# Kernel optimization log

Measured on AMD Instinct MI355X. Metric: run time of the kernel, lower is better.

The kernel has to match this reference:

```python
import jax, jax.numpy as jnp
import numpy as np
from jax import lax

HEADS = 4
DIM = 64
GATE_HID = 16


def setup_inputs() -> dict:
    key = jax.random.key(0)
    ks = jax.random.split(key, 12)
    b, c, h, w = 2, DIM, 48, 48
    s = 0.05
    x = jax.random.normal(ks[0], (b, c, h, w), jnp.float32)
    Wqkv = jax.random.normal(ks[1], (3 * c, c), jnp.float32) * s
    bqkv = jax.random.normal(ks[2], (3 * c,), jnp.float32) * s
    Wpos = jax.random.normal(ks[3], (3 * c, 1, 3, 3), jnp.float32) * s
    bpos = jax.random.normal(ks[4], (3 * c,), jnp.float32) * s
    Wg1 = jax.random.normal(ks[5], (GATE_HID, 1), jnp.float32) * 0.5
    bg1 = jax.random.normal(ks[6], (GATE_HID,), jnp.float32) * 0.1
    Wg2 = jax.random.normal(ks[7], (1, GATE_HID), jnp.float32) * 0.5
    bg2 = jax.random.normal(ks[8], (1,), jnp.float32) * 0.1
    Wproj = jax.random.normal(ks[9], (c, c), jnp.float32) * s
    bproj = jax.random.normal(ks[10], (c,), jnp.float32) * s
    return {"x": x, "Wqkv": Wqkv, "bqkv": bqkv, "Wpos": Wpos, "bpos": bpos,
            "Wg1": Wg1, "bg1": bg1, "Wg2": Wg2, "bg2": bg2,
            "Wproj": Wproj, "bproj": bproj}


def _forward(x, Wqkv, bqkv, Wpos, bpos, Wg1, bg1, Wg2, bg2, Wproj, bproj):
    b, c, h, w = x.shape
    n = h * w
    heads = HEADS
    hd = c // heads
    scale = hd ** -0.5
    # qkv 1x1 conv then 3x3 depthwise positional conv
    qkv = jnp.einsum('bchw,oc->bohw', x, Wqkv) + bqkv[None, :, None, None]
    qkv = lax.conv_general_dilated(
        qkv, Wpos, window_strides=(1, 1), padding='SAME',
        feature_group_count=3 * c,
        dimension_numbers=('NCHW', 'OIHW', 'NCHW')) + bpos[None, :, None, None]
    q, k, v = jnp.split(qkv, 3, axis=1)

    def to_heads(t):
        # [b,c,h,w] -> [b,heads,n,hd]
        return t.reshape(b, c, n).transpose(0, 2, 1).reshape(b, n, heads, hd).transpose(0, 2, 1, 3)

    q, k, v = to_heads(q), to_heads(k), to_heads(v)
    attn = jnp.einsum('bhid,bhjd->bhij', q, k) * scale  # [b,heads,n,n]
    prob = jax.nn.softmax(attn, axis=-1)
    entropy = -(prob * jnp.log(jnp.clip(prob, 1e-12))).sum(-1).mean(-1)  # [b,heads]
    # entropy gate: sigmoid(fc2(relu(fc1(e)))) * 0.9 + 0.1
    hgate = jax.nn.relu(entropy[..., None] @ Wg1.T + bg1)  # [b,heads,16]
    ratio = jax.nn.sigmoid(hgate @ Wg2.T + bg2)[..., 0] * 0.9 + 0.1  # [b,heads]
    # dynamic per-(batch,head) top-k along rows via rank threshold
    keep = jnp.clip(jnp.ceil(ratio * n).astype(jnp.int32), 1, n)  # [b,heads]
    sorted_desc = -jnp.sort(-attn, axis=-1)  # [b,heads,n,n]
    idx = jnp.broadcast_to((keep - 1)[:, :, None, None], (b, heads, n, 1))
    thresh = jnp.take_along_axis(sorted_desc, idx, axis=-1)  # [b,heads,n,1]
    sparse = jnp.where(attn >= thresh, attn, -jnp.inf)
    p = jax.nn.softmax(sparse, axis=-1)
    out = jnp.einsum('bhij,bhjd->bhid', p, v)  # [b,heads,n,hd]
    out = out.transpose(0, 2, 1, 3).reshape(b, n, c)
    out = out @ Wproj.T + bproj
    return out.transpose(0, 2, 1).reshape(b, c, h, w)


def reference(x, Wqkv, bqkv, Wpos, bpos, Wg1, bg1, Wg2, bg2, Wproj, bproj):
    return _forward(x, Wqkv, bqkv, Wpos, bpos, Wg1, bg1, Wg2, bg2, Wproj, bproj)
```

## Files before the change

kernel.cpp:

```cpp
#include <hip/hip_runtime.h>
#include <hip/hip_fp16.h>


#define NEG_INF (-__builtin_huge_valf())

typedef _Float16 half8_t __attribute__((ext_vector_type(8)));
typedef float floatx4 __attribute__((ext_vector_type(4)));

__device__ __forceinline__ unsigned h2key(unsigned short u) {
  return (u & 0x8000u) ? (unsigned)((~u) & 0xFFFFu) : (unsigned)(u | 0x8000u);
}
__device__ __forceinline__ float key16_to_float(unsigned k) {
  unsigned short u = (k & 0x8000u) ? (unsigned short)(k & 0x7FFFu)
                                   : (unsigned short)((~k) & 0xFFFFu);
  return __half2float(__ushort_as_half(u));
}

__device__ __forceinline__ float max8(uint4 v, float mx) {
  float2 f0 = __half22float2(*(__half2*)&v.x);
  float2 f1 = __half22float2(*(__half2*)&v.y);
  float2 f2 = __half22float2(*(__half2*)&v.z);
  float2 f3 = __half22float2(*(__half2*)&v.w);
  mx = fmaxf(mx, fmaxf(fmaxf(f0.x, f0.y), fmaxf(f1.x, f1.y)));
  mx = fmaxf(mx, fmaxf(fmaxf(f2.x, f2.y), fmaxf(f3.x, f3.y)));
  return mx;
}

__device__ __forceinline__ uint4 maskExp8(uint4 v, float th, float m,
                                          float& sp) {
  float2 f0 = __half22float2(*(__half2*)&v.x);
  float2 f1 = __half22float2(*(__half2*)&v.y);
  float2 f2 = __half22float2(*(__half2*)&v.z);
  float2 f3 = __half22float2(*(__half2*)&v.w);
  float p0 = (f0.x >= th) ? __expf(f0.x - m) : 0.f;
  float p1 = (f0.y >= th) ? __expf(f0.y - m) : 0.f;
  float p2 = (f1.x >= th) ? __expf(f1.x - m) : 0.f;
  float p3 = (f1.y >= th) ? __expf(f1.y - m) : 0.f;
  float p4 = (f2.x >= th) ? __expf(f2.x - m) : 0.f;
  float p5 = (f2.y >= th) ? __expf(f2.y - m) : 0.f;
  float p6 = (f3.x >= th) ? __expf(f3.x - m) : 0.f;
  float p7 = (f3.y >= th) ? __expf(f3.y - m) : 0.f;
  sp += ((p0 + p1) + (p2 + p3)) + ((p4 + p5) + (p6 + p7));
  uint4 o;
  __half2 h0 = __floats2half2_rn(p0, p1); o.x = *(unsigned*)&h0;
  __half2 h1 = __floats2half2_rn(p2, p3); o.y = *(unsigned*)&h1;
  __half2 h2 = __floats2half2_rn(p4, p5); o.z = *(unsigned*)&h2;
  __half2 h3 = __floats2half2_rn(p6, p7); o.w = *(unsigned*)&h3;
  return o;
}

__global__ __launch_bounds__(256) void k_qkv(const float* __restrict__ x,
                                             const float* __restrict__ W,
                                             const float* __restrict__ bias,
                                             float* __restrict__ out) {
  int blk = blockIdx.x;
  int chunk = blk % 9;
  int o = (blk / 9) % 192;
  int b = blk / (9 * 192);
  int pos = chunk * 256 + threadIdx.x;
  const float* xb = x + b * 64 * 2304 + pos;
  const float* wr = W + o * 64;
  float acc = bias[o];
#pragma unroll
  for (int c = 0; c < 64; c++) acc = fmaf(wr[c], xb[c * 2304], acc);
  out[(b * 192 + o) * 2304 + pos] = acc;
}

__global__ __launch_bounds__(256) void k_dw(const float* __restrict__ qkv,
                                            const float* __restrict__ Wpos,
                                            const float* __restrict__ bpos,
                                            _Float16* __restrict__ q2,
                                            _Float16* __restrict__ k2,
                                            _Float16* __restrict__ vt) {
  int blk = blockIdx.x;
  int chunk = blk % 9;
  int ch = (blk / 9) % 192;
  int b = blk / (9 * 192);
  int pos = chunk * 256 + threadIdx.x;
  int yy = pos / 48, xx = pos % 48;
  const float* in = qkv + (b * 192 + ch) * 2304;
  const float* w = Wpos + ch * 9;
  float acc = bpos[ch];
#pragma unroll
  for (int dy = -1; dy <= 1; dy++) {
    int y2 = yy + dy;
    if ((unsigned)y2 < 48u) {
#pragma unroll
      for (int dx = -1; dx <= 1; dx++) {
        int x2 = xx + dx;
        if ((unsigned)x2 < 48u)
          acc = fmaf(w[(dy + 1) * 3 + (dx + 1)], in[y2 * 48 + x2], acc);
      }
    }
  }
  int sel = ch >> 6;
  int c = ch & 63;
  int head = c >> 4, d = c & 15;
  int bh = b * 4 + head;
  if (sel == 2) {
    vt[((size_t)bh * 16 + d) * 2304 + pos] = (_Float16)acc;
  } else {
    if (sel == 0) acc *= 0.25f;
    size_t idx = (size_t)bh * 2304 + pos;
    _Float16 h1 = (_Float16)acc;
    float r = acc - (float)h1;
    _Float16 h2 = (_Float16)r;
    _Float16* dst = (sel == 0) ? q2 : k2;
    dst[idx * 32 + d] = h1;
    dst[idx * 32 + 16 + d] = h2;
  }
}

template <bool STORE>
__global__ __launch_bounds__(256) void k_ent_t(const _Float16* __restrict__ q2,
                                               const _Float16* __restrict__ k2,
                                               float* __restrict__ ent,
                                               _Float16* __restrict__ lgH) {
  __shared__ __align__(16) _Float16 tBuf[4][16][72];
  __shared__ float mWv[4][16], sWv[4][16], uWv[4][16];

  int blk = blockIdx.x;
  int rowtile = blk % 144;
  int bh = blk / 144;
  int row0 = rowtile * 16;
  int tid = threadIdx.x, lane = tid & 63, wave = tid >> 6;
  int m16 = lane & 15, quad = lane >> 4;

  const half8_t* q2v =
      (const half8_t*)(q2 + ((size_t)bh * 2304 + row0 + m16) * 32);
  half8_t A1 = q2v[quad];
  half8_t zh = {};
  half8_t A2 = (lane < 32) ? A1 : zh;
  const half8_t* kbase = (const half8_t*)(k2 + (size_t)bh * 2304 * 32);

  float mreg[4] = {NEG_INF, NEG_INF, NEG_INF, NEG_INF};
  for (int g = 0; g < 9; g++) {
#pragma unroll
    for (int tt = 0; tt < 4; tt++) {
      int t = g * 4 + tt;
      int col = wave * 576 + t * 16 + m16;
      const half8_t* kk = kbase + (size_t)col * 4;
      half8_t b1 = kk[quad & 1];
      half8_t b2 = kk[2 + (quad & 1)];
      floatx4 acc = {};
      acc = __builtin_amdgcn_mfma_f32_16x16x32_f16(A2, b2, acc, 0, 0, 0);
      acc = __builtin_amdgcn_mfma_f32_16x16x32_f16(A1, b1, acc, 0, 0, 0);
#pragma unroll
      for (int i = 0; i < 4; i++) {
        mreg[i] = fmaxf(mreg[i], acc[i]);
        if (STORE) tBuf[wave][quad * 4 + i][tt * 16 + m16] = (_Float16)acc[i];
      }
    }
    if (STORE) {
      __syncthreads();
      int rb = lane >> 3, seg = lane & 7;
#pragma unroll
      for (int it = 0; it < 2; it++) {
        int rr = it * 8 + rb;
        uint4 vv = *(const uint4*)&tBuf[wave][rr][seg * 8];
        *(uint4*)(lgH + ((size_t)bh * 2304 + row0 + rr) * 2304 + wave * 576 +
                  g * 64 + seg * 8) = vv;
      }
      __syncthreads();
    }
  }
#pragma unroll
  for (int off = 1; off < 16; off <<= 1)
#pragma unroll
    for (int i = 0; i < 4; i++)
      mreg[i] = fmaxf(mreg[i], __shfl_xor(mreg[i], off));
  if (m16 == 0) {
#pragma unroll
    for (int i = 0; i < 4; i++) mWv[wave][quad * 4 + i] = mreg[i];
  }
  __syncthreads();
  float mrow[4];
#pragma unroll
  for (int i = 0; i < 4; i++) {
    int r = quad * 4 + i;
    mrow[i] = fmaxf(fmaxf(mWv[0][r], mWv[1][r]), fmaxf(mWv[2][r], mWv[3][r]));
  }

  float s[4] = {0.f, 0.f, 0.f, 0.f}, u[4] = {0.f, 0.f, 0.f, 0.f};
#pragma unroll 4
  for (int t = 0; t < 36; t++) {
    int col = wave * 576 + t * 16 + m16;
    const half8_t* kk = kbase + (size_t)col * 4;
    half8_t b1 = kk[quad & 1];
    half8_t b2 = kk[2 + (quad & 1)];
    floatx4 acc = {};
    acc = __builtin_amdgcn_mfma_f32_16x16x32_f16(A2, b2, acc, 0, 0, 0);
    acc = __builtin_amdgcn_mfma_f32_16x16x32_f16(A1, b1, acc, 0, 0, 0);
#pragma unroll
    for (int i = 0; i < 4; i++) {
      float z = acc[i] - mrow[i];
      float e = __expf(z);
      s[i] += e;
      u[i] = fmaf(z, e, u[i]);
    }
  }
#pragma unroll
  for (int off = 1; off < 16; off <<= 1) {
#pragma unroll
    for (int i = 0; i < 4; i++) {
      s[i] += __shfl_xor(s[i], off);
      u[i] += __shfl_xor(u[i], off);
    }
  }
  if (m16 == 0) {
#pragma unroll
    for (int i = 0; i < 4; i++) {
      sWv[wave][quad * 4 + i] = s[i];
      uWv[wave][quad * 4 + i] = u[i];
    }
  }
  __syncthreads();
  if (tid < 16) {
    float S = sWv[0][tid] + sWv[1][tid] + sWv[2][tid] + sWv[3][tid];
    float U = uWv[0][tid] + uWv[1][tid] + uWv[2][tid] + uWv[3][tid];
    float er = __logf(S) - U / S;
    er += __shfl_xor(er, 1);
    er += __shfl_xor(er, 2);
    er += __shfl_xor(er, 4);
    er += __shfl_xor(er, 8);
    if (tid == 0) atomicAdd(&ent[bh], er);
  }
}

template <bool CACHED>
__global__ __launch_bounds__(256, 7) void k_attn_t(
    const _Float16* __restrict__ q2, const _Float16* __restrict__ k2,
    const _Float16* __restrict__ vt, const _Float16* __restrict__ lgH,
    const float* __restrict__ ent, const float* __restrict__ Wg1,
    const float* __restrict__ bg1, const float* __restrict__ Wg2,
    const float* __restrict__ bg2, float* __restrict__ oh) {
  __shared__ __align__(16) _Float16 pbuf[4][2320];
  __shared__ float sS[4];
  __shared__ float mShF[4][4];
  __shared__ __align__(16) float redSh[4][64];

  int blk = blockIdx.x;
  int rowblk = blk % 576;
  int bh = blk / 576;
  int row0 = rowblk * 4;
  int tid = threadIdx.x, lane = tid & 63, wave = tid >> 6;

  float eAvg = ent[bh] * (1.f / 2304.f);
  float gacc = bg2[0];
#pragma unroll
  for (int i = 0; i < 16; i++) {
    float h = fmaxf(fmaf(eAvg, Wg1[i], bg1[i]), 0.f);
    gacc = fmaf(h, Wg2[i], gacc);
  }
  float ratio = 0.9f / (1.f + __expf(-gacc)) + 0.1f;
  int kp = (int)ceilf(ratio * 2304.f);
  unsigned keep = (unsigned)min(max(kp, 1), 2304);

  float m;
  uint4* dst4 = (uint4*)pbuf[wave];
  if (CACHED) {
    const uint4* src =
        (const uint4*)(lgH + ((size_t)bh * 2304 + row0 + wave) * 2304);
    float mx = NEG_INF;
#pragma unroll
    for (int it = 0; it < 4; it++) {
      int idx = lane + it * 64;
      uint4 v = src[idx];
      dst4[idx] = v;
      mx = max8(v, mx);
    }
    if (lane < 32) {
      uint4 v = src[256 + lane];
      dst4[256 + lane] = v;
      mx = max8(v, mx);
    }
#pragma unroll
    for (int off = 1; off < 64; off <<= 1) mx = fmaxf(mx, __shfl_xor(mx, off));
    m = mx;
  } else {
    int m16 = lane & 15, quad = lane >> 4;
    const half8_t* q2v =
        (const half8_t*)(q2 + ((size_t)bh * 2304 + row0 + (m16 & 3)) * 32);
    half8_t A1 = q2v[quad];
    half8_t zh = {};
    half8_t A2 = (lane < 32) ? A1 : zh;
    const half8_t* kbase = (const half8_t*)(k2 + (size_t)bh * 2304 * 32);
    float ml[4] = {NEG_INF, NEG_INF, NEG_INF, NEG_INF};
#pragma unroll 4
    for (int t = 0; t < 36; t++) {
      int ct = wave * 36 + t;
      int col = ct * 16 + m16;
      const half8_t* kk = kbase + (size_t)col * 4;
      half8_t b1 = kk[quad & 1];
      half8_t b2 = kk[2 + (quad & 1)];
      floatx4 acc = {};
      acc = __builtin_amdgcn_mfma_f32_16x16x32_f16(A2, b2, acc, 0, 0, 0);
      acc = __builtin_amdgcn_mfma_f32_16x16x32_f16(A1, b1, acc, 0, 0, 0);
      if (lane < 16) {
#pragma unroll
        for (int i = 0; i < 4; i++) {
          pbuf[i][ct * 16 + lane] = (_Float16)acc[i];
          ml[i] = fmaxf(ml[i], acc[i]);
        }
      }
    }
#pragma unroll
    for (int off = 1; off < 16; off <<= 1)
#pragma unroll
      for (int i = 0; i < 4; i++) ml[i] = fmaxf(ml[i], __shfl_xor(ml[i], off));
    if (lane == 0) {
#pragma unroll
      for (int i = 0; i < 4; i++) mShF[wave][i] = ml[i];
    }
    __syncthreads();
    m = fmaxf(fmaxf(mShF[0][wave], mShF[1][wave]),
              fmaxf(mShF[2][wave], mShF[3][wave]));
  }

  float th;
  {
    const unsigned short* prow = (const unsigned short*)pbuf[wave];
    unsigned keys[36];
#pragma unroll
    for (int i = 0; i < 36; i++) keys[i] = h2key(prow[lane + i * 64]);
    unsigned T = 0u;
    for (int bit = 15; bit >= 0; --bit) {
      unsigned cand = T | (1u << bit);
      unsigned cnt = 0u;
#pragma unroll
      for (int i = 0; i < 36; i++)
        cnt += (unsigned)__popcll(__ballot(keys[i] >= cand));
      if (cnt >= keep) {
        T = cand;
        if (cnt == keep) break;
      }
    }
    th = key16_to_float(T);
  }

  {
    float sp = 0.f;
#pragma unroll
    for (int it = 0; it < 4; it++) {
      int idx = lane + it * 64;
      dst4[idx] = maskExp8(dst4[idx], th, m, sp);
    }
    if (lane < 32) {
      int idx = 256 + lane;
      dst4[idx] = maskExp8(dst4[idx], th, m, sp);
    }
#pragma unroll
    for (int off = 1; off < 64; off <<= 1) sp += __shfl_xor(sp, off);
    if (lane == 0) sS[wave] = sp;
  }
  __syncthreads();

  {
    int m16 = lane & 15, quad = lane >> 4;
    const _Float16* vrow = vt + ((size_t)bh * 16 + m16) * 2304;
    const _Float16* prow = pbuf[m16 & 3];
    int jb0 = wave * 576 + quad * 8;
    floatx4 acc = {};
#pragma unroll 6
    for (int t = 0; t < 18; t++) {
      int jb = jb0 + t * 32;
      half8_t a = *(const half8_t*)&prow[jb];
      half8_t b = *(const half8_t*)&vrow[jb];
      acc = __builtin_amdgcn_mfma_f32_16x16x32_f16(a, b, acc, 0, 0, 0);
    }
    if (lane < 16) {
      *(floatx4*)&redSh[wave][m16 * 4] = acc;
    }
  }
  __syncthreads();
  if (tid < 64) {
    int r = tid & 3, d = tid >> 2;
    float s2 = redSh[0][d * 4 + r] + redSh[1][d * 4 + r] +
               redSh[2][d * 4 + r] + redSh[3][d * 4 + r];
    oh[((size_t)(bh * 2304 + row0 + r)) * 16 + d] = s2 / sS[r];
  }
}

__global__ __launch_bounds__(256) void k_proj(const float* __restrict__ oh,
                                              const float* __restrict__ Wp,
                                              const float* __restrict__ bp,
                                              float* __restrict__ out) {
  int blk = blockIdx.x;
  int chunk = blk % 9;
  int co = (blk / 9) % 64;
  int b = blk / (9 * 64);
  int pos = chunk * 256 + threadIdx.x;
  const float* wr = Wp + co * 64;
  float acc = bp[co];
#pragma unroll
  for (int head = 0; head < 4; head++) {
    const float4* op =
        (const float4*)(oh + ((size_t)((b * 4 + head) * 2304 + pos)) * 16);
#pragma unroll
    for (int p = 0; p < 4; p++) {
      float4 o4 = op[p];
      acc = fmaf(wr[head * 16 + p * 4 + 0], o4.x, acc);
      acc = fmaf(wr[head * 16 + p * 4 + 1], o4.y, acc);
      acc = fmaf(wr[head * 16 + p * 4 + 2], o4.z, acc);
      acc = fmaf(wr[head * 16 + p * 4 + 3], o4.w, acc);
    }
  }
  out[(b * 64 + co) * 2304 + pos] = acc;
}

extern "C" void kernel_launch(void* const* d_in, const int* in_sizes, int n_in,
                              void* d_out, int out_size, void* d_ws,
                              size_t ws_size, hipStream_t stream) {
  const float* x    = (const float*)d_in[0];
  const float* Wqkv = (const float*)d_in[1];
  const float* bqkv = (const float*)d_in[2];
  const float* Wpos = (const float*)d_in[3];
  const float* bpos = (const float*)d_in[4];
  const float* Wg1  = (const float*)d_in[5];
  const float* bg1  = (const float*)d_in[6];
  const float* Wg2  = (const float*)d_in[7];
  const float* bg2  = (const float*)d_in[8];
  const float* Wpr  = (const float*)d_in[9];
  const float* bpr  = (const float*)d_in[10];
  float* out = (float*)d_out;

  const size_t lgBytes = (size_t)8 * 2304 * 2304 * 2;
  const size_t baseBytes = (size_t)(884736 + 294912 + 8) * 4 +
                           (size_t)(2 * 589824 + 294912) * 2;
  bool cached = ws_size >= lgBytes + baseBytes;

  char* base = (char*)d_ws;
  _Float16* lgH = nullptr;
  if (cached) {
    lgH = (_Float16*)base;
    base += lgBytes;
  }
  float* qkv_raw = (float*)base;
  float* oh = qkv_raw + 884736;
  float* ent = oh + 294912;
  _Float16* q2 = (_Float16*)(ent + 8);
  _Float16* k2 = q2 + 589824;
  _Float16* vt = k2 + 589824;

  (void)hipMemsetAsync(ent, 0, 8 * sizeof(float), stream);
  hipLaunchKernelGGL(k_qkv, dim3(2 * 192 * 9), dim3(256), 0, stream,
                     x, Wqkv, bqkv, qkv_raw);
  hipLaunchKernelGGL(k_dw, dim3(2 * 192 * 9), dim3(256), 0, stream,
                     qkv_raw, Wpos, bpos, q2, k2, vt);
  if (cached) {
    hipLaunchKernelGGL((k_ent_t<true>), dim3(8 * 144), dim3(256), 0, stream,
                       q2, k2, ent, lgH);
    hipLaunchKernelGGL((k_attn_t<true>), dim3(8 * 576), dim3(256), 0, stream,
                       q2, k2, vt, lgH, ent, Wg1, bg1, Wg2, bg2, oh);
  } else {
    hipLaunchKernelGGL((k_ent_t<false>), dim3(8 * 144), dim3(256), 0, stream,
                       q2, k2, ent, lgH);
    hipLaunchKernelGGL((k_attn_t<false>), dim3(8 * 576), dim3(256), 0, stream,
                       q2, k2, vt, lgH, ent, Wg1, bg1, Wg2, bg2, oh);
  }
  hipLaunchKernelGGL(k_proj, dim3(2 * 64 * 9), dim3(256), 0, stream,
                     oh, Wpr, bpr, out);
}
```

Before: 229.2 us.

## Register-block qkv/proj, tile depthwise conv in LDS, re-read cached logits for entropy

The qkv and projection kernels now compute four output channels per thread, so each loaded input value is reused four times and the grids shrink. The depthwise conv stages a 16-channel row tile in shared memory and writes each q/k position as vectorised 16-byte stores. The entropy memset is folded into the qkv kernel. In the cached path, the entropy pass now re-reads the just-written fp16 logits instead of recomputing them with a second MFMA sweep. The fp16 re-read slightly changes entropy precision, and the smaller grids may leave the GPU underfilled.

New measurement: 245.8 us. 1.07x slower.

```diff
diff --git a/kernel.cpp b/kernel.cpp
--- a/kernel.cpp
+++ b/kernel.cpp
@@ -52,18 +52,34 @@
 __global__ __launch_bounds__(256) void k_qkv(const float* __restrict__ x,
                                              const float* __restrict__ W,
                                              const float* __restrict__ bias,
-                                             float* __restrict__ out) {
+                                             float* __restrict__ out,
+                                             float* __restrict__ ent) {
+  if (blockIdx.x == 0 && threadIdx.x < 8) ent[threadIdx.x] = 0.f;
   int blk = blockIdx.x;
   int chunk = blk % 9;
-  int o = (blk / 9) % 192;
-  int b = blk / (9 * 192);
+  int og = (blk / 9) % 48;
+  int b = blk / (9 * 48);
+  int o0 = og * 4;
   int pos = chunk * 256 + threadIdx.x;
   const float* xb = x + b * 64 * 2304 + pos;
-  const float* wr = W + o * 64;
-  float acc = bias[o];
-#pragma unroll
-  for (int c = 0; c < 64; c++) acc = fmaf(wr[c], xb[c * 2304], acc);
-  out[(b * 192 + o) * 2304 + pos] = acc;
+  const float* w0 = W + (o0 + 0) * 64;
+  const float* w1 = W + (o0 + 1) * 64;
+  const float* w2 = W + (o0 + 2) * 64;
+  const float* w3 = W + (o0 + 3) * 64;
+  float a0 = bias[o0 + 0], a1 = bias[o0 + 1];
+  float a2 = bias[o0 + 2], a3 = bias[o0 + 3];
+#pragma unroll
+  for (int c = 0; c < 64; c++) {
+    float xv = xb[c * 2304];
+    a0 = fmaf(w0[c], xv, a0);
+    a1 = fmaf(w1[c], xv, a1);
+    a2 = fmaf(w2[c], xv, a2);
+    a3 = fmaf(w3[c], xv, a3);
+  }
+  out[(b * 192 + o0 + 0) * 2304 + pos] = a0;
+  out[(b * 192 + o0 + 1) * 2304 + pos] = a1;
+  out[(b * 192 + o0 + 2) * 2304 + pos] = a2;
+  out[(b * 192 + o0 + 3) * 2304 + pos] = a3;
 }
 
 __global__ __launch_bounds__(256) void k_dw(const float* __restrict__ qkv,
@@ -72,42 +88,73 @@
                                             _Float16* __restrict__ q2,
                                             _Float16* __restrict__ k2,
                                             _Float16* __restrict__ vt) {
+  __shared__ float smem[16][384];
   int blk = blockIdx.x;
   int chunk = blk % 9;
-  int ch = (blk / 9) % 192;
-  int b = blk / (9 * 192);
-  int pos = chunk * 256 + threadIdx.x;
-  int yy = pos / 48, xx = pos % 48;
-  const float* in = qkv + (b * 192 + ch) * 2304;
-  const float* w = Wpos + ch * 9;
-  float acc = bpos[ch];
-#pragma unroll
-  for (int dy = -1; dy <= 1; dy++) {
-    int y2 = yy + dy;
-    if ((unsigned)y2 < 48u) {
-#pragma unroll
-      for (int dx = -1; dx <= 1; dx++) {
-        int x2 = xx + dx;
-        if ((unsigned)x2 < 48u)
-          acc = fmaf(w[(dy + 1) * 3 + (dx + 1)], in[y2 * 48 + x2], acc);
-      }
-    }
-  }
-  int sel = ch >> 6;
-  int c = ch & 63;
-  int head = c >> 4, d = c & 15;
+  int sel = (blk / 9) % 3;
+  int head = (blk / 27) % 4;
+  int b = blk / 108;
+  int chbase = sel * 64 + head * 16;
   int bh = b * 4 + head;
+  int tid = threadIdx.x;
+  int p0 = chunk * 256;
+  int baserow = p0 / 48;
+  int rA = min(max(baserow - 1, 0), 40);
+
+  const float* src = qkv + (size_t)(b * 192 + chbase) * 2304;
+#pragma unroll
+  for (int l = 0; l < 24; l++) {
+    int idx = tid + l * 256;
+    int ch = idx / 384;
+    int off = idx - ch * 384;
+    int rr = off / 48;
+    int cc = off - rr * 48;
+    smem[ch][off] = src[(size_t)ch * 2304 + (rA + rr) * 48 + cc];
+  }
+  __syncthreads();
+
+  int pos = p0 + tid;
+  int yy = pos / 48, xx = pos - yy * 48;
+  int ry = yy - rA;
+  float accv[16];
+#pragma unroll
+  for (int d = 0; d < 16; d++) {
+    const float* w = Wpos + (chbase + d) * 9;
+    float a = bpos[chbase + d];
+#pragma unroll
+    for (int dy = -1; dy <= 1; dy++) {
+      int y2 = yy + dy;
+      if ((unsigned)y2 < 48u) {
+#pragma unroll
+        for (int dx = -1; dx <= 1; dx++) {
+          int x2 = xx + dx;
+          if ((unsigned)x2 < 48u)
+            a = fmaf(w[(dy + 1) * 3 + (dx + 1)], smem[d][(ry + dy) * 48 + x2],
+                     a);
+        }
+      }
+    }
+    accv[d] = a;
+  }
+
   if (sel == 2) {
-    vt[((size_t)bh * 16 + d) * 2304 + pos] = (_Float16)acc;
+#pragma unroll
+    for (int d = 0; d < 16; d++)
+      vt[((size_t)bh * 16 + d) * 2304 + pos] = (_Float16)accv[d];
   } else {
-    if (sel == 0) acc *= 0.25f;
-    size_t idx = (size_t)bh * 2304 + pos;
-    _Float16 h1 = (_Float16)acc;
-    float r = acc - (float)h1;
-    _Float16 h2 = (_Float16)r;
-    _Float16* dst = (sel == 0) ? q2 : k2;
-    dst[idx * 32 + d] = h1;
-    dst[idx * 32 + 16 + d] = h2;
+    _Float16 h1[16], h2[16];
+#pragma unroll
+    for (int d = 0; d < 16; d++) {
+      float a = (sel == 0) ? accv[d] * 0.25f : accv[d];
+      h1[d] = (_Float16)a;
+      h2[d] = (_Float16)(a - (float)h1[d]);
+    }
+    _Float16* dst = ((sel == 0) ? q2 : k2) + ((size_t)bh * 2304 + pos) * 32;
+    uint4* d4 = (uint4*)dst;
+    d4[0] = *(uint4*)&h1[0];
+    d4[1] = *(uint4*)&h1[8];
+    d4[2] = *(uint4*)&h2[0];
+    d4[3] = *(uint4*)&h2[8];
   }
 }
 
@@ -117,7 +164,9 @@
                                                float* __restrict__ ent,
                                                _Float16* __restrict__ lgH) {
   __shared__ __align__(16) _Float16 tBuf[4][16][72];
-  __shared__ float mWv[4][16], sWv[4][16], uWv[4][16];
+  __shared__ float mWv[4][16];
+  __shared__ float mFin[16];
+  __shared__ float sWv[4][16], uWv[4][16];
 
   int blk = blockIdx.x;
   int rowtile = blk % 144;
@@ -174,56 +223,96 @@
     for (int i = 0; i < 4; i++) mWv[wave][quad * 4 + i] = mreg[i];
   }
   __syncthreads();
-  float mrow[4];
-#pragma unroll
-  for (int i = 0; i < 4; i++) {
-    int r = quad * 4 + i;
-    mrow[i] = fmaxf(fmaxf(mWv[0][r], mWv[1][r]), fmaxf(mWv[2][r], mWv[3][r]));
-  }
-
-  float s[4] = {0.f, 0.f, 0.f, 0.f}, u[4] = {0.f, 0.f, 0.f, 0.f};
+  if (tid < 16) {
+    mFin[tid] = fmaxf(fmaxf(mWv[0][tid], mWv[1][tid]),
+                      fmaxf(mWv[2][tid], mWv[3][tid]));
+  }
+  __syncthreads();
+
+  if (STORE) {
+    float er_sum = 0.f;
+#pragma unroll
+    for (int rr = 0; rr < 4; rr++) {
+      int r = wave * 4 + rr;
+      float m = mFin[r];
+      const uint4* srcr =
+          (const uint4*)(lgH + ((size_t)bh * 2304 + row0 + r) * 2304);
+      float s = 0.f, u = 0.f;
+#pragma unroll
+      for (int it = 0; it < 5; it++) {
+        int idx = lane + it * 64;
+        if (it < 4 || lane < 32) {
+          uint4 v = srcr[idx];
+          float2 f0 = __half22float2(*(__half2*)&v.x);
+          float2 f1 = __half22float2(*(__half2*)&v.y);
+          float2 f2 = __half22float2(*(__half2*)&v.z);
+          float2 f3 = __half22float2(*(__half2*)&v.w);
+          float vals[8] = {f0.x, f0.y, f1.x, f1.y, f2.x, f2.y, f3.x, f3.y};
+#pragma unroll
+          for (int e = 0; e < 8; e++) {
+            float z = vals[e] - m;
+            float ev = __expf(z);
+            s += ev;
+            u = fmaf(z, ev, u);
+          }
+        }
+      }
+#pragma unroll
+      for (int off = 1; off < 64; off <<= 1) {
+        s += __shfl_xor(s, off);
+        u += __shfl_xor(u, off);
+      }
+      if (lane == 0) er_sum += __logf(s) - u / s;
+    }
+    if (lane == 0) atomicAdd(&ent[bh], er_sum);
+  } else {
+    float mrow[4];
+#pragma unroll
+    for (int i = 0; i < 4; i++) mrow[i] = mFin[quad * 4 + i];
+    float s[4] = {0.f, 0.f, 0.f, 0.f}, u[4] = {0.f, 0.f, 0.f, 0.f};
 #pragma unroll 4
-  for (int t = 0; t < 36; t++) {
-    int col = wave * 576 + t * 16 + m16;
-    const half8_t* kk = kbase + (size_t)col * 4;
-    half8_t b1 = kk[quad & 1];
-    half8_t b2 = kk[2 + (quad & 1)];
-    floatx4 acc = {};
-    acc = __builtin_amdgcn_mfma_f32_16x16x32_f16(A2, b2, acc, 0, 0, 0);
-    acc = __builtin_amdgcn_mfma_f32_16x16x32_f16(A1, b1, acc, 0, 0, 0);
-#pragma unroll
-    for (int i = 0; i < 4; i++) {
-      float z = acc[i] - mrow[i];
-      float e = __expf(z);
-      s[i] += e;
-      u[i] = fmaf(z, e, u[i]);
-    }
-  }
-#pragma unroll
-  for (int off = 1; off < 16; off <<= 1) {
-#pragma unroll
-    for (int i = 0; i < 4; i++) {
-      s[i] += __shfl_xor(s[i], off);
-      u[i] += __shfl_xor(u[i], off);
-    }
-  }
-  if (m16 == 0) {
-#pragma unroll
-    for (int i = 0; i < 4; i++) {
-      sWv[wave][quad * 4 + i] = s[i];
-      uWv[wave][quad * 4 + i] = u[i];
-    }
-  }
-  __syncthreads();
-  if (tid < 16) {
-    float S = sWv[0][tid] + sWv[1][tid] + sWv[2][tid] + sWv[3][tid];
-    float U = uWv[0][tid] + uWv[1][tid] + uWv[2][tid] + uWv[3][tid];
-    float er = __logf(S) - U / S;
-    er += __shfl_xor(er, 1);
-    er += __shfl_xor(er, 2);
-    er += __shfl_xor(er, 4);
-    er += __shfl_xor(er, 8);
-    if (tid == 0) atomicAdd(&ent[bh], er);
+    for (int t = 0; t < 36; t++) {
+      int col = wave * 576 + t * 16 + m16;
+      const half8_t* kk = kbase + (size_t)col * 4;
+      half8_t b1 = kk[quad & 1];
+      half8_t b2 = kk[2 + (quad & 1)];
+      floatx4 acc = {};
+      acc = __builtin_amdgcn_mfma_f32_16x16x32_f16(A2, b2, acc, 0, 0, 0);
+      acc = __builtin_amdgcn_mfma_f32_16x16x32_f16(A1, b1, acc, 0, 0, 0);
+#pragma unroll
+      for (int i = 0; i < 4; i++) {
+        float z = acc[i] - mrow[i];
+        float e = __expf(z);
+        s[i] += e;
+        u[i] = fmaf(z, e, u[i]);
+      }
+    }
+#pragma unroll
+    for (int off = 1; off < 16; off <<= 1) {
+#pragma unroll
+      for (int i = 0; i < 4; i++) {
+        s[i] += __shfl_xor(s[i], off);
+        u[i] += __shfl_xor(u[i], off);
+      }
+    }
+    if (m16 == 0) {
+#pragma unroll
+      for (int i = 0; i < 4; i++) {
+        sWv[wave][quad * 4 + i] = s[i];
+        uWv[wave][quad * 4 + i] = u[i];
+      }
+    }
+    __syncthreads();
+    if (tid < 16) {
+      float S = sWv[0][tid] + sWv[1][tid] + sWv[2][tid] + sWv[3][tid];
+      float U = uWv[0][tid] + uWv[1][tid] + uWv[2][tid] + uWv[3][tid];
+      float er = __logf(S) - U / S;
+      er += __shfl_xor(er, 1);
+      er += __shfl_xor(er, 2);
+      er += __shfl_xor(er, 4);
+      er += __shfl_xor(er, 8);
+      if (tid == 0) atomicAdd(&ent[bh], er);
+    }
   }
 }
 
@@ -387,11 +476,11 @@
                                               float* __restrict__ out) {
   int blk = blockIdx.x;
   int chunk = blk % 9;
-  int co = (blk / 9) % 64;
-  int b = blk / (9 * 64);
+  int cog = (blk / 9) % 16;
+  int b = blk / (9 * 16);
+  int co0 = cog * 4;
   int pos = chunk * 256 + threadIdx.x;
-  const float* wr = Wp + co * 64;
-  float acc = bp[co];
+  float a0 = bp[co0 + 0], a1 = bp[co0 + 1], a2 = bp[co0 + 2], a3 = bp[co0 + 3];
 #pragma unroll
   for (int head = 0; head < 4; head++) {
     const float4* op =
@@ -399,13 +488,21 @@
 #pragma unroll
     for (int p = 0; p < 4; p++) {
       float4 o4 = op[p];
-      acc = fmaf(wr[head * 16 + p * 4 + 0], o4.x, acc);
-      acc = fmaf(wr[head * 16 + p * 4 + 1], o4.y, acc);
-      acc = fmaf(wr[head * 16 + p * 4 + 2], o4.z, acc);
-      acc = fmaf(wr[head * 16 + p * 4 + 3], o4.w, acc);
-    }
-  }
-  out[(b * 64 + co) * 2304 + pos] = acc;
+#pragma unroll
+      for (int i = 0; i < 4; i++) {
+        const float* wr = Wp + (co0 + i) * 64 + head * 16 + p * 4;
+        float* ai = (i == 0) ? &a0 : ((i == 1) ? &a1 : ((i == 2) ? &a2 : &a3));
+        *ai = fmaf(wr[0], o4.x, *ai);
+        *ai = fmaf(wr[1], o4.y, *ai);
+        *ai = fmaf(wr[2], o4.z, *ai);
+        *ai = fmaf(wr[3], o4.w, *ai);
+      }
+    }
+  }
+  out[(b * 64 + co0 + 0) * 2304 + pos] = a0;
+  out[(b * 64 + co0 + 1) * 2304 + pos] = a1;
+  out[(b * 64 + co0 + 2) * 2304 + pos] = a2;
+  out[(b * 64 + co0 + 3) * 2304 + pos] = a3;
 }
 
 extern "C" void kernel_launch(void* const* d_in, const int* in_sizes, int n_in,
@@ -442,10 +539,9 @@
   _Float16* k2 = q2 + 589824;
   _Float16* vt = k2 + 589824;
 
-  (void)hipMemsetAsync(ent, 0, 8 * sizeof(float), stream);
-  hipLaunchKernelGGL(k_qkv, dim3(2 * 192 * 9), dim3(256), 0, stream,
-                     x, Wqkv, bqkv, qkv_raw);
-  hipLaunchKernelGGL(k_dw, dim3(2 * 192 * 9), dim3(256), 0, stream,
+  hipLaunchKernelGGL(k_qkv, dim3(2 * 48 * 9), dim3(256), 0, stream,
+                     x, Wqkv, bqkv, qkv_raw, ent);
+  hipLaunchKernelGGL(k_dw, dim3(216), dim3(256), 0, stream,
                      qkv_raw, Wpos, bpos, q2, k2, vt);
   if (cached) {
     hipLaunchKernelGGL((k_ent_t<true>), dim3(8 * 144), dim3(256), 0, stream,
@@ -458,6 +554,6 @@
     hipLaunchKernelGGL((k_attn_t<false>), dim3(8 * 576), dim3(256), 0, stream,
                        q2, k2, vt, lgH, ent, Wg1, bg1, Wg2, bg2, oh);
   }
-  hipLaunchKernelGGL(k_proj, dim3(2 * 64 * 9), dim3(256), 0, stream,
+  hipLaunchKernelGGL(k_proj, dim3(2 * 16 * 9), dim3(256), 0, stream,
                      oh, Wpr, bpr, out);
 }
```
